# Performance work log

Hardware: AMD Instinct MI355X
Metric: run time of the kernel (lower is better)

The kernel has to match this reference:

```python
import jax, jax.numpy as jnp
import numpy as np

BEV_H, BEV_W = 496, 432  # cfg.bevshape

def mish(x):
    return x * jnp.tanh(jax.nn.softplus(x))

def ln(x, g, b, eps=1e-5):
    m = jnp.mean(x, axis=-1, keepdims=True)
    v = jnp.mean((x - m) ** 2, axis=-1, keepdims=True)
    return (x - m) * jax.lax.rsqrt(v + eps) * g + b

def fel(x, W, g, b):
    # FELayer: Linear(bias=False) -> LayerNorm -> Mish
    return mish(ln(x @ W.T, g, b))

def setup_inputs() -> dict:
    key = jax.random.key(0)
    ks = iter(jax.random.split(key, 48))
    Nv, P, Cin, Cv, Nb = 16000, 32, 10, 64, 16000
    inp = {}
    inp['voxels'] = jax.random.normal(next(ks), (Nv, P, Cin), jnp.float32)
    inp['voxelmask'] = jax.random.bernoulli(next(ks), 0.7, (Nv, P, 1)).astype(jnp.float32)
    inp['bevsidx'] = jax.random.randint(next(ks), (Nb, 64), 0, Nv, dtype=jnp.int32)
    flat = jax.random.choice(next(ks), BEV_H * BEV_W, (Nb,), replace=False)
    inp['bevcoors'] = jnp.stack([flat // BEV_W, flat % BEV_W], axis=1).astype(jnp.int32)
    inp['bevmask'] = jax.random.bernoulli(next(ks), 0.8, (Nb, 1, 1)).astype(jnp.float32)
    def w(shape):
        return jax.random.normal(next(ks), shape, jnp.float32) * 0.05
    for i, cin in zip((1, 2, 3, 4), (Cin, Cv, Cv, Cv)):
        inp[f'vfe{i}_W'] = w((Cv, cin))
        inp[f'vfe{i}_g'] = jnp.ones((Cv,), jnp.float32)
        inp[f'vfe{i}_b'] = jnp.zeros((Cv,), jnp.float32)
    inp['bfe1_W'] = w((16, Cv, Cv));  inp['bfe1_g'] = jnp.ones((16, Cv));  inp['bfe1_b'] = jnp.zeros((16, Cv))
    inp['bfe2a_W'] = w((16, 8, Cv)); inp['bfe2a_g'] = jnp.ones((16, 8));  inp['bfe2a_b'] = jnp.zeros((16, 8))
    inp['bfe2b_W'] = w((16, 8, 32)); inp['bfe2b_g'] = jnp.ones((16, 8));  inp['bfe2b_b'] = jnp.zeros((16, 8))
    inp['bfe3_W'] = w((128, 128));   inp['bfe3_g'] = jnp.ones((128,));   inp['bfe3_b'] = jnp.zeros((128,))
    return inp

def reference(voxels, voxelmask, bevsidx, bevcoors, bevmask,
              vfe1_W, vfe1_g, vfe1_b, vfe2_W, vfe2_g, vfe2_b,
              vfe3_W, vfe3_g, vfe3_b, vfe4_W, vfe4_g, vfe4_b,
              bfe1_W, bfe1_g, bfe1_b, bfe2a_W, bfe2a_g, bfe2a_b,
              bfe2b_W, bfe2b_g, bfe2b_b, bfe3_W, bfe3_g, bfe3_b):
    # voxel feature encoder with masked residual
    x1 = fel(voxels, vfe1_W, vfe1_g, vfe1_b)            # [Nv, P, 64]
    x2 = fel(x1, vfe2_W, vfe2_g, vfe2_b) * voxelmask
    x3 = fel(x2, vfe3_W, vfe3_g, vfe3_b)
    x4 = fel(x3, vfe4_W, vfe4_g, vfe4_b) * voxelmask + x2
    voxelwise = jnp.max(x4, axis=1)                     # [Nv, 64]
    # gather 64 voxels per BEV cell
    bevs = voxelwise[bevsidx]                           # [Nb, 64 voxels, 64 ch]
    x0 = jnp.transpose(bevs, (0, 2, 1))                 # [Nb, 64 ch, 64 voxels]
    Nb = x0.shape[0]
    xg = x0.reshape(Nb, 16, 4, 64)                      # 16 branches of 4 channel-rows
    # bfe1_k (vectorized over the 16 branches) + bev mask
    h = mish(ln(jnp.einsum('ngpc,goc->ngpo', xg, bfe1_W), bfe1_g[:, None, :], bfe1_b[:, None, :]))
    h = h * bevmask[:, None]                            # bevmask [Nb,1,1] -> broadcast
    # bfe2_k: NormalFELayer(in_points=4, in=64, out=8)
    h = mish(ln(jnp.einsum('ngpc,goc->ngpo', h, bfe2a_W), bfe2a_g[:, None, :], bfe2a_b[:, None, :]))
    h = h.reshape(Nb, 16, 32)
    h = mish(ln(jnp.einsum('ngc,goc->ngo', h, bfe2b_W), bfe2b_g, bfe2b_b))  # [Nb,16,8]
    x17 = h.reshape(Nb, 128)                            # cat of 16 branches
    x18 = fel(x17, bfe3_W, bfe3_g, bfe3_b)
    x19 = fel(x18, bfe3_W, bfe3_g, bfe3_b) + x17        # same bfe3 applied twice + residual
    bevmap = jnp.zeros((BEV_H, BEV_W, 128), jnp.float32).at[bevcoors[:, 0], bevcoors[:, 1]].set(x19)
    return jnp.transpose(bevmap, (2, 1, 0))             # [128, W, H]
```

## Files before the change

### kernel.cpp

```cpp
#include <hip/hip_runtime.h>
#include <math.h>

constexpr int NV  = 16000;
constexpr int P   = 32;
constexpr int CIN = 10;
constexpr int CV  = 64;
constexpr int NB  = 16000;
constexpr int BEV_H = 496, BEV_W = 432;
constexpr int HW = BEV_H * BEV_W;
constexpr float EPS = 1e-5f;

typedef __attribute__((ext_vector_type(8))) short short8_t;
typedef __attribute__((ext_vector_type(4))) short short4_t;
typedef __attribute__((ext_vector_type(4))) float fx4;
typedef __attribute__((ext_vector_type(2))) float f32x2;

__device__ __forceinline__ float mish(float x) {
  float e = __expf(fminf(x, 15.f));
  float u = 1.f + e;
  float d = fmaf(u, u, 1.f);
  float r = __builtin_amdgcn_rcpf(d);
  return fmaf(-2.f * x, r, x);
}

__device__ __forceinline__ short f2bf(float f) {
  unsigned u = __builtin_bit_cast(unsigned, f);
  u += 0x7FFF + ((u >> 16) & 1);
  return (short)(u >> 16);
}
__device__ __forceinline__ float bf2f(short s) {
  unsigned u = ((unsigned)(unsigned short)s) << 16;
  return __builtin_bit_cast(float, u);
}
__device__ __forceinline__ short8_t pack8(const float* t) {
  short8_t s;
#pragma unroll
  for (int j = 0; j < 8; ++j) s[j] = f2bf(t[j]);
  return s;
}

__device__ __forceinline__ unsigned bfpair(float a, float b) {
  unsigned au = __builtin_bit_cast(unsigned, a) + 0x8000u;
  unsigned bu = __builtin_bit_cast(unsigned, b) + 0x8000u;
  return __builtin_amdgcn_perm(bu, au, 0x07060302u);
}
__device__ __forceinline__ unsigned hipack(float a, float b, float& la, float& lb) {
  unsigned ua = (__builtin_bit_cast(unsigned, a) + 0x8000u) & 0xFFFF0000u;
  unsigned ub = (__builtin_bit_cast(unsigned, b) + 0x8000u) & 0xFFFF0000u;
  la = a - __builtin_bit_cast(float, ua);
  lb = b - __builtin_bit_cast(float, ub);
  return __builtin_amdgcn_perm(ub, ua, 0x07060302u);
}

__global__ __launch_bounds__(256) void pack_weights_kernel(
    const float* __restrict__ W1, const float* __restrict__ W2a,
    const float* __restrict__ W2b, const float* __restrict__ W3,
    short* __restrict__ w1h, short* __restrict__ w1l,
    short* __restrict__ w2ah, short* __restrict__ w2al,
    short* __restrict__ w2bh, short* __restrict__ w2bl,
    short* __restrict__ w3h, short* __restrict__ w3l)
{
  int i = blockIdx.x * 256 + threadIdx.x;
  if (i < 65536) {
    float v = W1[i];
    short h = f2bf(v);
    w1h[i] = h; w1l[i] = f2bf(v - bf2f(h));
  } else if (i < 81920) {
    int j = i - 65536;
    int g = j >> 10, o = (j >> 6) & 15, c = j & 63;
    float v = (o < 8) ? W2a[(g * 8 + o) * 64 + c] : 0.f;
    short h = f2bf(v);
    w2ah[j] = h; w2al[j] = f2bf(v - bf2f(h));
  } else if (i < 90112) {
    int k = i - 81920;
    int g = k >> 9, o = (k >> 5) & 15, c = k & 31;
    float v = (o < 8) ? W2b[(g * 8 + o) * 32 + c] : 0.f;
    short h = f2bf(v);
    w2bh[k] = h; w2bl[k] = f2bf(v - bf2f(h));
  } else if (i < 106496) {
    int j = i - 90112;
    float v = W3[j];
    short h = f2bf(v);
    w3h[j] = h; w3l[j] = f2bf(v - bf2f(h));
  }
}

__global__ __launch_bounds__(256, 4) void vfe_mfma4_kernel(
    const float* __restrict__ voxels, const float* __restrict__ vmask,
    const float* __restrict__ W1, const float* __restrict__ g1, const float* __restrict__ b1,
    const float* __restrict__ W2, const float* __restrict__ g2, const float* __restrict__ b2,
    const float* __restrict__ W3, const float* __restrict__ g3, const float* __restrict__ b3,
    const float* __restrict__ W4, const float* __restrict__ g4, const float* __restrict__ b4,
    float* __restrict__ voxelwise)
{
  __shared__ short wlds[28 * 512];
  __shared__ short actb[4][16 * 72];
  __shared__ float gblds[512];

  const int tid  = threadIdx.x;
  const int lane = tid & 63;
  const int w    = tid >> 6;
  const int p    = lane & 15;
  const int q    = lane >> 4;
  const int gw   = blockIdx.x * 4 + w;

  for (int k = tid; k < 512; k += 256) {
    int region = k >> 6, off = k & 63;
    const float* src =
        region == 0 ? g1 : region == 1 ? b1 :
        region == 2 ? g2 : region == 3 ? b2 :
        region == 4 ? g3 : region == 5 ? b3 :
        region == 6 ? g4 : b4;
    gblds[k] = src[off];
  }
  for (int s = w; s < 28; s += 4) {
    float t[8];
    if (s < 4) {
      const int f = s;
#pragma unroll
      for (int j = 0; j < 8; ++j) {
        int c = 8 * q + j;
        t[j] = (c < CIN) ? W1[(p + 16 * f) * CIN + c] : 0.f;
      }
    } else {
      const int l = (s - 4) >> 3, rem = (s - 4) & 7, ch = rem >> 2, f = rem & 3;
      const float* Wl = (l == 0) ? W2 : (l == 1) ? W3 : W4;
      const float* src = Wl + (p + 16 * f) * CV + 32 * ch + 8 * q;
#pragma unroll
      for (int j = 0; j < 8; ++j) t[j] = src[j];
    }
    *(short8_t*)&wlds[s * 512 + lane * 8] = pack8(t);
  }
  __syncthreads();

  short* mybuf = &actb[w][0];
  const fx4 zacc = {0.f, 0.f, 0.f, 0.f};
  const int srcLane = ((lane >> 2) & 3) * 16 + (((lane >> 4) & 3) << 2) + (lane & 3);

  for (int i = 0; i < 4; ++i) {
    const int v = gw * 4 + i;
    float chmax0 = 0.f, vmaxv = 0.f;

    for (int h = 0; h < 2; ++h) {
      const int ptbase = v * 32 + h * 16;
      const float m = vmask[ptbase + p];
      float x2r[16];
      float cur[16];

      {
        const float* xrow = voxels + (size_t)(ptbase + p) * CIN;
        float t[8] = {0.f, 0.f, 0.f, 0.f, 0.f, 0.f, 0.f, 0.f};
        if (q == 0) {
          float2 a = *(const float2*)(xrow + 0);
          float2 b = *(const float2*)(xrow + 2);
          float2 c = *(const float2*)(xrow + 4);
          float2 d = *(const float2*)(xrow + 6);
          t[0] = a.x; t[1] = a.y; t[2] = b.x; t[3] = b.y;
          t[4] = c.x; t[5] = c.y; t[6] = d.x; t[7] = d.y;
        } else if (q == 1) {
          float2 a = *(const float2*)(xrow + 8);
          t[0] = a.x; t[1] = a.y;
        }
        uint4 bu = make_uint4(bfpair(t[0], t[1]), bfpair(t[2], t[3]),
                              bfpair(t[4], t[5]), bfpair(t[6], t[7]));
        short8_t bfrag = __builtin_bit_cast(short8_t, bu);
        fx4 acc[4];
#pragma unroll
        for (int f = 0; f < 4; ++f) {
          short8_t af = *(short8_t*)&wlds[f * 512 + lane * 8];
          acc[f] = __builtin_amdgcn_mfma_f32_16x16x32_bf16(af, bfrag, zacc, 0, 0, 0);
        }
        f32x2 s1v = {0.f, 0.f}, s2v = {0.f, 0.f};
#pragma unroll
        for (int f = 0; f < 4; ++f) {
          f32x2 a01 = __builtin_shufflevector(acc[f], acc[f], 0, 1);
          f32x2 a23 = __builtin_shufflevector(acc[f], acc[f], 2, 3);
          s1v = s1v + a01 + a23;
          s2v = __builtin_elementwise_fma(a01, a01, s2v);
          s2v = __builtin_elementwise_fma(a23, a23, s2v);
        }
        float s1 = s1v[0] + s1v[1], s2 = s2v[0] + s2v[1];
        s1 += __shfl_xor(s1, 16); s1 += __shfl_xor(s1, 32);
        s2 += __shfl_xor(s2, 16); s2 += __shfl_xor(s2, 32);
        float mean = s1 * (1.f / 64.f);
        float rstd = rsqrtf(fmaf(-mean, mean, s2 * (1.f / 64.f)) + EPS);
        float ms = -mean * rstd;
#pragma unroll
        for (int f = 0; f < 4; ++f) {
          float4 gv = *(const float4*)&gblds[0 * 128 + 16 * f + 4 * q];
          float4 bv = *(const float4*)&gblds[0 * 128 + 64 + 16 * f + 4 * q];
          float go[4] = {gv.x, gv.y, gv.z, gv.w};
          float bo[4] = {bv.x, bv.y, bv.z, bv.w};
          float o[4];
#pragma unroll
          for (int r = 0; r < 4; ++r)
            o[r] = mish(fmaf(fmaf(acc[f][r], rstd, ms), go[r], bo[r]));
          *(uint2*)&mybuf[p * 72 + 4 * q + 16 * f] =
              make_uint2(bfpair(o[0], o[1]), bfpair(o[2], o[3]));
        }
      }

#pragma unroll 1
      for (int l = 0; l < 3; ++l) {
        short8_t bf0 = *(short8_t*)&mybuf[p * 72 + 8 * q];
        short8_t bf1 = *(short8_t*)&mybuf[p * 72 + 8 * q + 32];
        fx4 acc[4];
#pragma unroll
        for (int f = 0; f < 4; ++f) {
          short8_t a0 = *(short8_t*)&wlds[(4 + l * 8 + f) * 512 + lane * 8];
          short8_t a1 = *(short8_t*)&wlds[(4 + l * 8 + 4 + f) * 512 + lane * 8];
          fx4 a = __builtin_amdgcn_mfma_f32_16x16x32_bf16(a0, bf0, zacc, 0, 0, 0);
          acc[f] = __builtin_amdgcn_mfma_f32_16x16x32_bf16(a1, bf1, a, 0, 0, 0);
        }
        f32x2 s1v = {0.f, 0.f}, s2v = {0.f, 0.f};
#pragma unroll
        for (int f = 0; f < 4; ++f) {
          f32x2 a01 = __builtin_shufflevector(acc[f], acc[f], 0, 1);
          f32x2 a23 = __builtin_shufflevector(acc[f], acc[f], 2, 3);
          s1v = s1v + a01 + a23;
          s2v = __builtin_elementwise_fma(a01, a01, s2v);
          s2v = __builtin_elementwise_fma(a23, a23, s2v);
        }
        float s1 = s1v[0] + s1v[1], s2 = s2v[0] + s2v[1];
        s1 += __shfl_xor(s1, 16); s1 += __shfl_xor(s1, 32);
        s2 += __shfl_xor(s2, 16); s2 += __shfl_xor(s2, 32);
        float mean = s1 * (1.f / 64.f);
        float rstd = rsqrtf(fmaf(-mean, mean, s2 * (1.f / 64.f)) + EPS);
        float ms = -mean * rstd;
        const int gbbase = (l + 1) * 128;
#pragma unroll
        for (int f = 0; f < 4; ++f) {
          float4 gv = *(const float4*)&gblds[gbbase + 16 * f + 4 * q];
          float4 bv = *(const float4*)&gblds[gbbase + 64 + 16 * f + 4 * q];
          float go[4] = {gv.x, gv.y, gv.z, gv.w};
          float bo[4] = {bv.x, bv.y, bv.z, bv.w};
          if (l == 0) {
            float o[4];
#pragma unroll
            for (int r = 0; r < 4; ++r) {
              o[r] = mish(fmaf(fmaf(acc[f][r], rstd, ms), go[r], bo[r])) * m;
              x2r[f * 4 + r] = o[r];
            }
            *(uint2*)&mybuf[p * 72 + 4 * q + 16 * f] =
                make_uint2(bfpair(o[0], o[1]), bfpair(o[2], o[3]));
          } else if (l == 1) {
            float o[4];
#pragma unroll
            for (int r = 0; r < 4; ++r)
              o[r] = mish(fmaf(fmaf(acc[f][r], rstd, ms), go[r], bo[r]));
            *(uint2*)&mybuf[p * 72 + 4 * q + 16 * f] =
                make_uint2(bfpair(o[0], o[1]), bfpair(o[2], o[3]));
          } else {
#pragma unroll
            for (int r = 0; r < 4; ++r) {
              float t1 = fmaf(fmaf(acc[f][r], rstd, ms), go[r], bo[r]);
              cur[f * 4 + r] = fmaf(mish(t1), m, x2r[f * 4 + r]);
            }
          }
        }
      }

#pragma unroll
      for (int t = 0; t < 8; ++t) {
        float send = (lane & 8) ? cur[t] : cur[t + 8];
        float got  = __shfl_xor(send, 8);
        float mine = (lane & 8) ? cur[t + 8] : cur[t];
        cur[t] = fmaxf(mine, got);
      }
#pragma unroll
      for (int t = 0; t < 4; ++t) {
        float send = (lane & 4) ? cur[t] : cur[t + 4];
        float got  = __shfl_xor(send, 4);
        float mine = (lane & 4) ? cur[t + 4] : cur[t];
        cur[t] = fmaxf(mine, got);
      }
#pragma unroll
      for (int t = 0; t < 2; ++t) {
        float send = (lane & 2) ? cur[t] : cur[t + 2];
        float got  = __shfl_xor(send, 2);
        float mine = (lane & 2) ? cur[t + 2] : cur[t];
        cur[t] = fmaxf(mine, got);
      }
      {
        float send = (lane & 1) ? cur[0] : cur[1];
        float got  = __shfl_xor(send, 1);
        float mine = (lane & 1) ? cur[1] : cur[0];
        cur[0] = fmaxf(mine, got);
      }
      float hm = __shfl(cur[0], srcLane);
      if (h == 0) chmax0 = hm; else vmaxv = fmaxf(chmax0, hm);
    }
    voxelwise[v * 64 + lane] = vmaxv;
  }
}

constexpr int XS_CH   = 72;
constexpr int XS_CELL = 16 * 72 + 16;
constexpr int ACT_OFF = 8 * XS_CELL;
constexpr int ACT_WS  = 16 * 72;
constexpr int H2_OFF  = ACT_OFF + 4 * ACT_WS;
constexpr int H2_WS   = 16 * 40;
constexpr int SMEM_SHORTS = H2_OFF + 4 * H2_WS;

__global__ __launch_bounds__(256, 4) void bfe12_mfma3_kernel(
    const float* __restrict__ voxelwise, const int* __restrict__ bevsidx,
    const float* __restrict__ bevmask,
    const short* __restrict__ w1h,
    const float* __restrict__ g1, const float* __restrict__ b1,
    const short* __restrict__ w2ah,
    const float* __restrict__ g2a, const float* __restrict__ b2a,
    const short* __restrict__ w2bh,
    const float* __restrict__ g2b, const float* __restrict__ b2b,
    float* __restrict__ x17buf)
{
  extern __shared__ short sm[];

  const int tid  = threadIdx.x;
  const int lane = tid & 63;
  const int w    = tid >> 6;
  const int r15  = lane & 15;
  const int q    = lane >> 4;
  const int cellbase = blockIdx.x * 8;

  const int chq   = lane & 3;
  const int v_loc = (lane >> 2) & 3;
  const int vblk  = lane >> 4;
  const int bit0  = v_loc & 1, bit1 = v_loc >> 1;

  int idxr[2][4];
#pragma unroll
  for (int cc = 0; cc < 2; ++cc)
#pragma unroll
    for (int vb = 0; vb < 4; ++vb) {
      int v = 16 * vb + 4 * vblk + v_loc;
      idxr[cc][vb] = bevsidx[(cellbase + 2 * w + cc) * 64 + v];
    }

  {
    short* zh = &sm[H2_OFF + w * H2_WS];
    for (int i = lane; i < 320; i += 64) zh[320 + i] = 0;
  }

  const fx4 zacc = {0.f, 0.f, 0.f, 0.f};
  short* acth = &sm[ACT_OFF + w * ACT_WS];
  short* h2h  = &sm[H2_OFF + w * H2_WS];

#pragma unroll 1
  for (int j = 0; j < 4; ++j) {
    const int g = 4 * j + w;

    __syncthreads();

#pragma unroll
    for (int cc = 0; cc < 2; ++cc) {
#pragma unroll
      for (int vb = 0; vb < 4; ++vb) {
        const float* src = voxelwise + (size_t)idxr[cc][vb] * 64 + 16 * j + 4 * chq;
        float4 f4 = *(const float4*)src;
        float a0 = f4.x, a1 = f4.y, a2 = f4.z, a3 = f4.w;
        float gv0 = bit0 ? a0 : a1, gv1 = bit0 ? a2 : a3;
        float r0 = __shfl_xor(gv0, 4), r1 = __shfl_xor(gv1, 4);
        float c0 = bit0 ? r0 : a0, c1 = bit0 ? a1 : r0;
        float c2 = bit0 ? r1 : a2, c3 = bit0 ? a3 : r1;
        float h0 = bit1 ? c0 : c2, h1 = bit1 ? c1 : c3;
        float s0 = __shfl_xor(h0, 8), s1 = __shfl_xor(h1, 8);
        float d0 = bit1 ? s0 : c0, d1 = bit1 ? s1 : c1;
        float d2 = bit1 ? c2 : s0, d3 = bit1 ? c3 : s1;
        int addr = (2 * w + cc) * XS_CELL + (4 * chq + v_loc) * XS_CH + 16 * vb + 4 * vblk;
        *(uint2*)&sm[addr] = make_uint2(bfpair(d0, d1), bfpair(d2, d3));
      }
    }

    __syncthreads();

    short8_t W1f[2][4];
#pragma unroll
    for (int c = 0; c < 2; ++c)
#pragma unroll
      for (int f = 0; f < 4; ++f) {
        int off = (g * 64 + r15 + 16 * f) * 64 + 32 * c + 8 * q;
        W1f[c][f] = *(const short8_t*)&w1h[off];
      }
    short8_t W2af[2];
#pragma unroll
    for (int c = 0; c < 2; ++c) {
      int off = (g * 16 + r15) * 64 + 32 * c + 8 * q;
      W2af[c] = *(const short8_t*)&w2ah[off];
    }
    short8_t W2bf;
    {
      int off = (g * 16 + r15) * 32 + 8 * q;
      W2bf = *(const short8_t*)&w2bh[off];
    }

#pragma unroll 1
    for (int t = 0; t < 2; ++t) {
      const int cl = r15 >> 2, p = r15 & 3;
      const int cell_loc = 4 * t + cl;
      const float bm = bevmask[cellbase + cell_loc];

      int xaddr = cell_loc * XS_CELL + (4 * w + p) * XS_CH;
      short8_t x0 = *(short8_t*)&sm[xaddr + 8 * q];
      short8_t x1 = *(short8_t*)&sm[xaddr + 32 + 8 * q];

      fx4 acc[4];
#pragma unroll
      for (int f = 0; f < 4; ++f) {
        fx4 a = __builtin_amdgcn_mfma_f32_16x16x32_bf16(W1f[0][f], x0, zacc, 0, 0, 0);
        acc[f] = __builtin_amdgcn_mfma_f32_16x16x32_bf16(W1f[1][f], x1, a, 0, 0, 0);
      }

      f32x2 s1v = {0.f, 0.f}, s2v = {0.f, 0.f};
#pragma unroll
      for (int f = 0; f < 4; ++f) {
        f32x2 a01 = __builtin_shufflevector(acc[f], acc[f], 0, 1);
        f32x2 a23 = __builtin_shufflevector(acc[f], acc[f], 2, 3);
        s1v = s1v + a01 + a23;
        s2v = __builtin_elementwise_fma(a01, a01, s2v);
        s2v = __builtin_elementwise_fma(a23, a23, s2v);
      }
      float s1 = s1v[0] + s1v[1], s2 = s2v[0] + s2v[1];
      s1 += __shfl_xor(s1, 16); s1 += __shfl_xor(s1, 32);
      s2 += __shfl_xor(s2, 16); s2 += __shfl_xor(s2, 32);
      float mean = s1 * (1.f / 64.f);
      float rstd = rsqrtf(fmaf(-mean, mean, s2 * (1.f / 64.f)) + EPS);
      float ms = -mean * rstd;

#pragma unroll
      for (int f = 0; f < 4; ++f) {
        float4 gv = *(const float4*)(g1 + g * 64 + 16 * f + 4 * q);
        float4 bv = *(const float4*)(b1 + g * 64 + 16 * f + 4 * q);
        float go[4] = {gv.x, gv.y, gv.z, gv.w};
        float bo[4] = {bv.x, bv.y, bv.z, bv.w};
        float o[4];
#pragma unroll
        for (int r = 0; r < 4; ++r)
          o[r] = mish(fmaf(fmaf(acc[f][r], rstd, ms), go[r], bo[r])) * bm;
        *(uint2*)&acth[r15 * 72 + 16 * f + 4 * q] =
            make_uint2(bfpair(o[0], o[1]), bfpair(o[2], o[3]));
      }

      short8_t a0 = *(short8_t*)&acth[r15 * 72 + 8 * q];
      short8_t a1 = *(short8_t*)&acth[r15 * 72 + 32 + 8 * q];
      fx4 a2 = __builtin_amdgcn_mfma_f32_16x16x32_bf16(W2af[0], a0, zacc, 0, 0, 0);
      a2 = __builtin_amdgcn_mfma_f32_16x16x32_bf16(W2af[1], a1, a2, 0, 0, 0);

      float sa = a2[0] + a2[1] + a2[2] + a2[3];
      float sb = fmaf(a2[0], a2[0], fmaf(a2[1], a2[1], fmaf(a2[2], a2[2], a2[3] * a2[3])));
      sa += __shfl_xor(sa, 16); sb += __shfl_xor(sb, 16);
      if (q < 2) {
        float mean2 = sa * 0.125f;
        float rstd2 = rsqrtf(fmaf(-mean2, mean2, sb * 0.125f) + EPS);
        float ms2 = -mean2 * rstd2;
        float4 gv = *(const float4*)(g2a + g * 8 + 4 * q);
        float4 bv = *(const float4*)(b2a + g * 8 + 4 * q);
        float go[4] = {gv.x, gv.y, gv.z, gv.w};
        float bo[4] = {bv.x, bv.y, bv.z, bv.w};
        float o[4];
#pragma unroll
        for (int r = 0; r < 4; ++r)
          o[r] = mish(fmaf(fmaf(a2[r], rstd2, ms2), go[r], bo[r]));
        *(uint2*)&h2h[cell_loc * 40 + p * 8 + 4 * q] =
            make_uint2(bfpair(o[0], o[1]), bfpair(o[2], o[3]));
      }
    }

    {
      short8_t bh = *(short8_t*)&h2h[r15 * 40 + 8 * q];
      fx4 a3 = __builtin_amdgcn_mfma_f32_16x16x32_bf16(W2bf, bh, zacc, 0, 0, 0);

      float sa = a3[0] + a3[1] + a3[2] + a3[3];
      float sb = fmaf(a3[0], a3[0], fmaf(a3[1], a3[1], fmaf(a3[2], a3[2], a3[3] * a3[3])));
      sa += __shfl_xor(sa, 16); sb += __shfl_xor(sb, 16);
      if (q < 2 && r15 < 8) {
        float mean3 = sa * 0.125f;
        float rstd3 = rsqrtf(fmaf(-mean3, mean3, sb * 0.125f) + EPS);
        float ms3 = -mean3 * rstd3;
        float4 gv = *(const float4*)(g2b + g * 8 + 4 * q);
        float4 bv = *(const float4*)(b2b + g * 8 + 4 * q);
        float go[4] = {gv.x, gv.y, gv.z, gv.w};
        float bo[4] = {bv.x, bv.y, bv.z, bv.w};
        float4 outv;
        float* op = &outv.x;
#pragma unroll
        for (int r = 0; r < 4; ++r)
          op[r] = mish(fmaf(fmaf(a3[r], rstd3, ms3), go[r], bo[r]));
        *(float4*)&x17buf[(size_t)(cellbase + r15) * 128 + g * 8 + 4 * q] = outv;
      }
    }
  }
}

__global__ __launch_bounds__(256, 2) void bfe3_mfma2_kernel(
    const float* __restrict__ x17buf, const int* __restrict__ bevcoors,
    const short* __restrict__ w3h, const short* __restrict__ w3l,
    const float* __restrict__ g3, const float* __restrict__ b3,
    float* __restrict__ out)
{
  __shared__ short x18h[4][16 * 136];
  __shared__ short x18l[4][16 * 136];

  const int tid  = threadIdx.x;
  const int lane = tid & 63;
  const int w    = tid >> 6;
  const int r15  = lane & 15;
  const int q    = lane >> 4;
  const int cell = blockIdx.x * 64 + w * 16 + r15;
  const float* xr = x17buf + (size_t)cell * 128;
  short* xh18 = &x18h[w][0];
  short* xl18 = &x18l[w][0];
  const fx4 zacc = {0.f, 0.f, 0.f, 0.f};

  short8_t xh[4], xl[4];
#pragma unroll
  for (int c = 0; c < 4; ++c) {
    const float* s = xr + 32 * c + 8 * q;
    float4 A = *(const float4*)s;
    float4 B = *(const float4*)(s + 4);
    float t[8] = {A.x, A.y, A.z, A.w, B.x, B.y, B.z, B.w};
    unsigned hu[4], lu[4];
#pragma unroll
    for (int jj = 0; jj < 4; ++jj) {
      float la, lb;
      hu[jj] = hipack(t[2 * jj], t[2 * jj + 1], la, lb);
      lu[jj] = bfpair(la, lb);
    }
    xh[c] = __builtin_bit_cast(short8_t, make_uint4(hu[0], hu[1], hu[2], hu[3]));
    xl[c] = __builtin_bit_cast(short8_t, make_uint4(lu[0], lu[1], lu[2], lu[3]));
  }

  fx4 acc[8];
#pragma unroll
  for (int f = 0; f < 8; ++f) {
    fx4 a = zacc;
#pragma unroll
    for (int c = 0; c < 4; ++c) {
      int off = (16 * f + r15) * 128 + 32 * c + 8 * q;
      short8_t Ah = *(const short8_t*)&w3h[off];
      short8_t Al = *(const short8_t*)&w3l[off];
      a = __builtin_amdgcn_mfma_f32_16x16x32_bf16(Ah, xh[c], a, 0, 0, 0);
      a = __builtin_amdgcn_mfma_f32_16x16x32_bf16(Ah, xl[c], a, 0, 0, 0);
      a = __builtin_amdgcn_mfma_f32_16x16x32_bf16(Al, xh[c], a, 0, 0, 0);
    }
    acc[f] = a;
  }
  {
    f32x2 s1v = {0.f, 0.f}, s2v = {0.f, 0.f};
#pragma unroll
    for (int f = 0; f < 8; ++f) {
      f32x2 a01 = __builtin_shufflevector(acc[f], acc[f], 0, 1);
      f32x2 a23 = __builtin_shufflevector(acc[f], acc[f], 2, 3);
      s1v = s1v + a01 + a23;
      s2v = __builtin_elementwise_fma(a01, a01, s2v);
      s2v = __builtin_elementwise_fma(a23, a23, s2v);
    }
    float s1 = s1v[0] + s1v[1], s2 = s2v[0] + s2v[1];
    s1 += __shfl_xor(s1, 16); s1 += __shfl_xor(s1, 32);
    s2 += __shfl_xor(s2, 16); s2 += __shfl_xor(s2, 32);
    float mean = s1 * (1.f / 128.f);
    float rstd = rsqrtf(fmaf(-mean, mean, s2 * (1.f / 128.f)) + EPS);
    float ms = -mean * rstd;
#pragma unroll
    for (int f = 0; f < 8; ++f) {
      float4 gv = *(const float4*)(g3 + 16 * f + 4 * q);
      float4 bv = *(const float4*)(b3 + 16 * f + 4 * q);
      float go[4] = {gv.x, gv.y, gv.z, gv.w};
      float bo[4] = {bv.x, bv.y, bv.z, bv.w};
      float o[4];
#pragma unroll
      for (int r = 0; r < 4; ++r)
        o[r] = mish(fmaf(fmaf(acc[f][r], rstd, ms), go[r], bo[r]));
      float la0, lb0, la1, lb1;
      unsigned h01 = hipack(o[0], o[1], la0, lb0);
      unsigned h23 = hipack(o[2], o[3], la1, lb1);
      *(uint2*)&xh18[r15 * 136 + 16 * f + 4 * q] = make_uint2(h01, h23);
      *(uint2*)&xl18[r15 * 136 + 16 * f + 4 * q] =
          make_uint2(bfpair(la0, lb0), bfpair(la1, lb1));
    }
  }

  short8_t yh[4], yl[4];
#pragma unroll
  for (int c = 0; c < 4; ++c) {
    yh[c] = *(short8_t*)&xh18[r15 * 136 + 32 * c + 8 * q];
    yl[c] = *(short8_t*)&xl18[r15 * 136 + 32 * c + 8 * q];
  }
#pragma unroll
  for (int f = 0; f < 8; ++f) {
    fx4 a = zacc;
#pragma unroll
    for (int c = 0; c < 4; ++c) {
      int off = (16 * f + r15) * 128 + 32 * c + 8 * q;
      short8_t Ah = *(const short8_t*)&w3h[off];
      short8_t Al = *(const short8_t*)&w3l[off];
      a = __builtin_amdgcn_mfma_f32_16x16x32_bf16(Ah, yh[c], a, 0, 0, 0);
      a = __builtin_amdgcn_mfma_f32_16x16x32_bf16(Ah, yl[c], a, 0, 0, 0);
      a = __builtin_amdgcn_mfma_f32_16x16x32_bf16(Al, yh[c], a, 0, 0, 0);
    }
    acc[f] = a;
  }
  {
    f32x2 s1v = {0.f, 0.f}, s2v = {0.f, 0.f};
#pragma unroll
    for (int f = 0; f < 8; ++f) {
      f32x2 a01 = __builtin_shufflevector(acc[f], acc[f], 0, 1);
      f32x2 a23 = __builtin_shufflevector(acc[f], acc[f], 2, 3);
      s1v = s1v + a01 + a23;
      s2v = __builtin_elementwise_fma(a01, a01, s2v);
      s2v = __builtin_elementwise_fma(a23, a23, s2v);
    }
    float s1 = s1v[0] + s1v[1], s2 = s2v[0] + s2v[1];
    s1 += __shfl_xor(s1, 16); s1 += __shfl_xor(s1, 32);
    s2 += __shfl_xor(s2, 16); s2 += __shfl_xor(s2, 32);
    float mean = s1 * (1.f / 128.f);
    float rstd = rsqrtf(fmaf(-mean, mean, s2 * (1.f / 128.f)) + EPS);
    float ms = -mean * rstd;

    int2 hw2 = *(const int2*)&bevcoors[cell * 2];
    const int base = hw2.y * BEV_H + hw2.x;
#pragma unroll
    for (int f = 0; f < 8; ++f) {
      float4 gv = *(const float4*)(g3 + 16 * f + 4 * q);
      float4 bv = *(const float4*)(b3 + 16 * f + 4 * q);
      float go[4] = {gv.x, gv.y, gv.z, gv.w};
      float bo[4] = {bv.x, bv.y, bv.z, bv.w};
      float4 R = *(const float4*)(xr + 16 * f + 4 * q);
      float Ra[4] = {R.x, R.y, R.z, R.w};
#pragma unroll
      for (int r = 0; r < 4; ++r) {
        float t1 = fmaf(fmaf(acc[f][r], rstd, ms), go[r], bo[r]);
        float val = mish(t1) + Ra[r];
        out[(size_t)(16 * f + 4 * q + r) * HW + base] = val;
      }
    }
  }
}

extern "C" void kernel_launch(void* const* d_in, const int* in_sizes, int n_in,
                              void* d_out, int out_size, void* d_ws, size_t ws_size,
                              hipStream_t stream) {
  const float* voxels   = (const float*)d_in[0];
  const float* vmask    = (const float*)d_in[1];
  const int*   bevsidx  = (const int*)d_in[2];
  const int*   bevcoors = (const int*)d_in[3];
  const float* bevmask  = (const float*)d_in[4];
  const float* vfe1_W = (const float*)d_in[5];
  const float* vfe1_g = (const float*)d_in[6];
  const float* vfe1_b = (const float*)d_in[7];
  const float* vfe2_W = (const float*)d_in[8];
  const float* vfe2_g = (const float*)d_in[9];
  const float* vfe2_b = (const float*)d_in[10];
  const float* vfe3_W = (const float*)d_in[11];
  const float* vfe3_g = (const float*)d_in[12];
  const float* vfe3_b = (const float*)d_in[13];
  const float* vfe4_W = (const float*)d_in[14];
  const float* vfe4_g = (const float*)d_in[15];
  const float* vfe4_b = (const float*)d_in[16];
  const float* bfe1_W  = (const float*)d_in[17];
  const float* bfe1_g  = (const float*)d_in[18];
  const float* bfe1_b  = (const float*)d_in[19];
  const float* bfe2a_W = (const float*)d_in[20];
  const float* bfe2a_g = (const float*)d_in[21];
  const float* bfe2a_b = (const float*)d_in[22];
  const float* bfe2b_W = (const float*)d_in[23];
  const float* bfe2b_g = (const float*)d_in[24];
  const float* bfe2b_b = (const float*)d_in[25];
  const float* bfe3_W  = (const float*)d_in[26];
  const float* bfe3_g  = (const float*)d_in[27];
  const float* bfe3_b  = (const float*)d_in[28];

  float* voxelwise = (float*)d_ws;
  float* x17buf    = voxelwise + NV * CV;
  short* wbase     = (short*)(x17buf + (size_t)NB * 128);
  short* w1h  = wbase;
  short* w1l  = w1h + 65536;
  short* w2ah = w1l + 65536;
  short* w2al = w2ah + 16384;
  short* w2bh = w2al + 16384;
  short* w2bl = w2bh + 8192;
  short* w3h  = w2bl + 8192;
  short* w3l  = w3h + 16384;
  float* out = (float*)d_out;

  hipMemsetAsync(d_out, 0, (size_t)out_size * sizeof(float), stream);

  pack_weights_kernel<<<(106496 + 255) / 256, 256, 0, stream>>>(
      bfe1_W, bfe2a_W, bfe2b_W, bfe3_W,
      w1h, w1l, w2ah, w2al, w2bh, w2bl, w3h, w3l);

  vfe_mfma4_kernel<<<NV / 16, 256, 0, stream>>>(
      voxels, vmask,
      vfe1_W, vfe1_g, vfe1_b, vfe2_W, vfe2_g, vfe2_b,
      vfe3_W, vfe3_g, vfe3_b, vfe4_W, vfe4_g, vfe4_b,
      voxelwise);

  bfe12_mfma3_kernel<<<NB / 8, 256, SMEM_SHORTS * sizeof(short), stream>>>(
      voxelwise, bevsidx, bevmask,
      w1h, bfe1_g, bfe1_b,
      w2ah, bfe2a_g, bfe2a_b,
      w2bh, bfe2b_g, bfe2b_b,
      x17buf);

  bfe3_mfma2_kernel<<<NB / 64, 256, 0, stream>>>(
      x17buf, bevcoors, w3h, w3l, bfe3_g, bfe3_b, out);
}
```

Measured before the change: 429.8 us.

## Store voxelwise features as bf16, stage x17 in LDS, drop unused low weights

The voxel encoder now writes its max-pooled features as rounded bf16 instead of fp32, which halves the storage and the gather traffic in the BEV kernel. The BEV kernel reads those bf16 values and unpacks them to floats. It also stages its x17 output in shared memory and then writes it back in coalesced full rows. Weight packing no longer produces the low-half bf16 parts that were never used for W1/W2a/W2b, and bfe3 launch bounds are raised to 3 blocks per CU. The voxelwise values already fed bf16 MFMAs, so precision should barely change, though the rounding now happens before the transpose/gather instead of inside it.

```diff
diff --git a/kernel.cpp b/kernel.cpp
--- a/kernel.cpp
+++ b/kernel.cpp
@@ -55,28 +55,24 @@
 __global__ __launch_bounds__(256) void pack_weights_kernel(
     const float* __restrict__ W1, const float* __restrict__ W2a,
     const float* __restrict__ W2b, const float* __restrict__ W3,
-    short* __restrict__ w1h, short* __restrict__ w1l,
-    short* __restrict__ w2ah, short* __restrict__ w2al,
-    short* __restrict__ w2bh, short* __restrict__ w2bl,
+    short* __restrict__ w1h,
+    short* __restrict__ w2ah,
+    short* __restrict__ w2bh,
     short* __restrict__ w3h, short* __restrict__ w3l)
 {
   int i = blockIdx.x * 256 + threadIdx.x;
   if (i < 65536) {
-    float v = W1[i];
-    short h = f2bf(v);
-    w1h[i] = h; w1l[i] = f2bf(v - bf2f(h));
+    w1h[i] = f2bf(W1[i]);
   } else if (i < 81920) {
     int j = i - 65536;
     int g = j >> 10, o = (j >> 6) & 15, c = j & 63;
     float v = (o < 8) ? W2a[(g * 8 + o) * 64 + c] : 0.f;
-    short h = f2bf(v);
-    w2ah[j] = h; w2al[j] = f2bf(v - bf2f(h));
+    w2ah[j] = f2bf(v);
   } else if (i < 90112) {
     int k = i - 81920;
     int g = k >> 9, o = (k >> 5) & 15, c = k & 31;
     float v = (o < 8) ? W2b[(g * 8 + o) * 32 + c] : 0.f;
-    short h = f2bf(v);
-    w2bh[k] = h; w2bl[k] = f2bf(v - bf2f(h));
+    w2bh[k] = f2bf(v);
   } else if (i < 106496) {
     int j = i - 90112;
     float v = W3[j];
@@ -85,13 +81,13 @@
   }
 }
 
-__global__ __launch_bounds__(256, 4) void vfe_mfma4_kernel(
+__global__ __launch_bounds__(256, 4) void vfe_mfma5_kernel(
     const float* __restrict__ voxels, const float* __restrict__ vmask,
     const float* __restrict__ W1, const float* __restrict__ g1, const float* __restrict__ b1,
     const float* __restrict__ W2, const float* __restrict__ g2, const float* __restrict__ b2,
     const float* __restrict__ W3, const float* __restrict__ g3, const float* __restrict__ b3,
     const float* __restrict__ W4, const float* __restrict__ g4, const float* __restrict__ b4,
-    float* __restrict__ voxelwise)
+    unsigned short* __restrict__ voxelwise)
 {
   __shared__ short wlds[28 * 512];
   __shared__ short actb[4][16 * 72];
@@ -187,8 +183,8 @@
         float ms = -mean * rstd;
 #pragma unroll
         for (int f = 0; f < 4; ++f) {
-          float4 gv = *(const float4*)&gblds[0 * 128 + 16 * f + 4 * q];
-          float4 bv = *(const float4*)&gblds[0 * 128 + 64 + 16 * f + 4 * q];
+          float4 gv = *(const float4*)&gblds[16 * f + 4 * q];
+          float4 bv = *(const float4*)&gblds[64 + 16 * f + 4 * q];
           float go[4] = {gv.x, gv.y, gv.z, gv.w};
           float bo[4] = {bv.x, bv.y, bv.z, bv.w};
           float o[4];
@@ -290,7 +286,8 @@
       float hm = __shfl(cur[0], srcLane);
       if (h == 0) chmax0 = hm; else vmaxv = fmaxf(chmax0, hm);
     }
-    voxelwise[v * 64 + lane] = vmaxv;
+    unsigned uv = __builtin_bit_cast(unsigned, vmaxv) + 0x8000u;
+    voxelwise[v * 64 + lane] = (unsigned short)(uv >> 16);
   }
 }
 
@@ -300,10 +297,11 @@
 constexpr int ACT_WS  = 16 * 72;
 constexpr int H2_OFF  = ACT_OFF + 4 * ACT_WS;
 constexpr int H2_WS   = 16 * 40;
-constexpr int SMEM_SHORTS = H2_OFF + 4 * H2_WS;
-
-__global__ __launch_bounds__(256, 4) void bfe12_mfma3_kernel(
-    const float* __restrict__ voxelwise, const int* __restrict__ bevsidx,
+constexpr int X17_OFF = H2_OFF + 4 * H2_WS;
+constexpr int SMEM_SHORTS = X17_OFF + 8 * 132 * 2;
+
+__global__ __launch_bounds__(256, 4) void bfe12_mfma4_kernel(
+    const unsigned short* __restrict__ voxelwise, const int* __restrict__ bevsidx,
     const float* __restrict__ bevmask,
     const short* __restrict__ w1h,
     const float* __restrict__ g1, const float* __restrict__ b1,
@@ -314,6 +312,7 @@
     float* __restrict__ x17buf)
 {
   extern __shared__ short sm[];
+  float* x17lds = (float*)&sm[X17_OFF];
 
   const int tid  = threadIdx.x;
   const int lane = tid & 63;
@@ -355,9 +354,13 @@
     for (int cc = 0; cc < 2; ++cc) {
 #pragma unroll
       for (int vb = 0; vb < 4; ++vb) {
-        const float* src = voxelwise + (size_t)idxr[cc][vb] * 64 + 16 * j + 4 * chq;
-        float4 f4 = *(const float4*)src;
-        float a0 = f4.x, a1 = f4.y, a2 = f4.z, a3 = f4.w;
+        const unsigned short* src =
+            voxelwise + (size_t)idxr[cc][vb] * 64 + 16 * j + 4 * chq;
+        uint2 u2 = *(const uint2*)src;
+        float a0 = __builtin_bit_cast(float, u2.x << 16);
+        float a1 = __builtin_bit_cast(float, u2.x & 0xFFFF0000u);
+        float a2 = __builtin_bit_cast(float, u2.y << 16);
+        float a3 = __builtin_bit_cast(float, u2.y & 0xFFFF0000u);
         float gv0 = bit0 ? a0 : a1, gv1 = bit0 ? a2 : a3;
         float r0 = __shfl_xor(gv0, 4), r1 = __shfl_xor(gv1, 4);
         float c0 = bit0 ? r0 : a0, c1 = bit0 ? a1 : r0;
@@ -485,13 +488,21 @@
 #pragma unroll
         for (int r = 0; r < 4; ++r)
           op[r] = mish(fmaf(fmaf(a3[r], rstd3, ms3), go[r], bo[r]));
-        *(float4*)&x17buf[(size_t)(cellbase + r15) * 128 + g * 8 + 4 * q] = outv;
-      }
-    }
-  }
-}
-
-__global__ __launch_bounds__(256, 2) void bfe3_mfma2_kernel(
+        *(float4*)&x17lds[r15 * 132 + g * 8 + 4 * q] = outv;
+      }
+    }
+  }
+
+  __syncthreads();
+  {
+    const int cell = tid >> 5;
+    const int off  = (tid & 31) * 4;
+    float4 vq = *(const float4*)&x17lds[cell * 132 + off];
+    *(float4*)&x17buf[(size_t)(cellbase + cell) * 128 + off] = vq;
+  }
+}
+
+__global__ __launch_bounds__(256, 3) void bfe3_mfma2_kernel(
     const float* __restrict__ x17buf, const int* __restrict__ bevcoors,
     const short* __restrict__ w3h, const short* __restrict__ w3l,
     const float* __restrict__ g3, const float* __restrict__ b3,
@@ -669,16 +680,13 @@
   const float* bfe3_g  = (const float*)d_in[27];
   const float* bfe3_b  = (const float*)d_in[28];
 
-  float* voxelwise = (float*)d_ws;
-  float* x17buf    = voxelwise + NV * CV;
-  short* wbase     = (short*)(x17buf + (size_t)NB * 128);
+  unsigned short* voxelwise = (unsigned short*)d_ws;
+  float* x17buf = (float*)(voxelwise + (size_t)NV * 64);
+  short* wbase  = (short*)(x17buf + (size_t)NB * 128);
   short* w1h  = wbase;
-  short* w1l  = w1h + 65536;
-  short* w2ah = w1l + 65536;
-  short* w2al = w2ah + 16384;
-  short* w2bh = w2al + 16384;
-  short* w2bl = w2bh + 8192;
-  short* w3h  = w2bl + 8192;
+  short* w2ah = w1h + 65536;
+  short* w2bh = w2ah + 16384;
+  short* w3h  = w2bh + 8192;
   short* w3l  = w3h + 16384;
   float* out = (float*)d_out;
 
@@ -686,15 +694,15 @@
 
   pack_weights_kernel<<<(106496 + 255) / 256, 256, 0, stream>>>(
       bfe1_W, bfe2a_W, bfe2b_W, bfe3_W,
-      w1h, w1l, w2ah, w2al, w2bh, w2bl, w3h, w3l);
-
-  vfe_mfma4_kernel<<<NV / 16, 256, 0, stream>>>(
+      w1h, w2ah, w2bh, w3h, w3l);
+
+  vfe_mfma5_kernel<<<NV / 16, 256, 0, stream>>>(
       voxels, vmask,
       vfe1_W, vfe1_g, vfe1_b, vfe2_W, vfe2_g, vfe2_b,
       vfe3_W, vfe3_g, vfe3_b, vfe4_W, vfe4_g, vfe4_b,
       voxelwise);
 
-  bfe12_mfma3_kernel<<<NB / 8, 256, SMEM_SHORTS * sizeof(short), stream>>>(
+  bfe12_mfma4_kernel<<<NB / 8, 256, SMEM_SHORTS * sizeof(short), stream>>>(
       voxelwise, bevsidx, bevmask,
       w1h, bfe1_g, bfe1_b,
       w2ah, bfe2a_g, bfe2a_b,
```

Result: no change. 433.4 us (+0.8%).
